# Optimization experiments

Measured on AMD Instinct MI355X. Metric: run time of the kernel, lower is better.

## Reference

```python
import jax, jax.numpy as jnp
import numpy as np

ALPHA = 1.0

def _soft_assign(x, clusters, alpha=ALPHA):
    # (avoids materializing the (N, K, D) broadcast intermediate)
    x_sq = jnp.sum(x * x, axis=1, keepdims=True)            # (N, 1)
    c_sq = jnp.sum(clusters * clusters, axis=1)             # (K,)
    cross = jnp.einsum('nd,kd->nk', x, clusters)            # (N, K)
    dist_sq = jnp.maximum(x_sq + c_sq[None, :] - 2.0 * cross, 0.0)
    q = 1.0 / (1.0 + dist_sq / alpha)
    q = q ** ((alpha + 1.0) / 2.0)
    return q / jnp.sum(q, axis=1, keepdims=True)            # row-normalize

def setup_inputs() -> dict:
    key = jax.random.key(0)
    k1, k2 = jax.random.split(key)
    N, D, K = 65536, 512, 1024
    x = jax.random.normal(k1, (N, D), dtype=jnp.float32)
    # xavier_uniform for (K, D): limit = sqrt(6 / (K + D))
    limit = float(np.sqrt(6.0 / (K + D)))
    clusters = jax.random.uniform(k2, (K, D), dtype=jnp.float32, minval=-limit, maxval=limit)
    return {"x": x, "clusters": clusters}

def reference(x, clusters):
    return _soft_assign(x, clusters)
```

## Files before the change

kernel.cpp:

```cpp
#include <hip/hip_runtime.h>

typedef __bf16 bf16x8 __attribute__((ext_vector_type(8)));
typedef float f32x16 __attribute__((ext_vector_type(16)));

__device__ __forceinline__ unsigned short f2bf(float f) {
    unsigned int u = __float_as_uint(f);
    u += 0x7FFFu + ((u >> 16) & 1u);
    return (unsigned short)(u >> 16);
}

__global__ __launch_bounds__(256) void prep_clusters(
    const float* __restrict__ cl, unsigned short* __restrict__ cbf,
    float* __restrict__ csq) {
    const int row  = blockIdx.x * 4 + (threadIdx.x >> 6);
    const int lane = threadIdx.x & 63;
    const float4* cg = (const float4*)(cl + ((size_t)row << 9));
    float ssq = 0.f;
#pragma unroll
    for (int i = 0; i < 2; ++i) {
        float4 v = cg[lane + 64 * i];
        ssq += v.x * v.x + v.y * v.y + v.z * v.z + v.w * v.w;
        ushort4 h;
        h.x = f2bf(v.x); h.y = f2bf(v.y); h.z = f2bf(v.z); h.w = f2bf(v.w);
        *(ushort4*)(cbf + ((size_t)row << 9) + (size_t)(lane + 64 * i) * 4) = h;
    }
#pragma unroll
    for (int off = 32; off >= 1; off >>= 1) ssq += __shfl_xor(ssq, off);
    if (lane == 0) csq[row] = ssq;
}

#define LDA 272

__global__ __launch_bounds__(1024, 4) void soft_assign(
    const float* __restrict__ x, const unsigned short* __restrict__ cbf,
    const float* __restrict__ csq, float* __restrict__ out) {
    __shared__ unsigned short xs[64 * LDA];
    __shared__ float part[64 * 32];
    __shared__ float xsq[64];
    __shared__ float inv[64];

    const int t    = threadIdx.x;
    const int lane = t & 63;
    const int w    = t >> 6;
    const int l31  = lane & 31;
    const int half = lane >> 5;
    const int rb   = blockIdx.x;

    part[t] = 0.f;
    part[t + 1024] = 0.f;

    const int col0   = w * 64 + l31;
    const float csq0 = csq[col0];
    const float csq1 = csq[col0 + 32];

    f32x16 c00, c01, c10, c11;
#pragma unroll
    for (int i = 0; i < 16; ++i) { c00[i] = 0.f; c01[i] = 0.f; c10[i] = 0.f; c11[i] = 0.f; }

    const int srow = t >> 4;
    const int sj   = t & 15;
    float ssq = 0.f;

    const unsigned short* b0base = cbf + (size_t)col0 * 512 + half * 8;
    const unsigned short* b1base = b0base + 32 * 512;
    const unsigned short* a0base = xs + l31 * LDA + half * 8;
    const unsigned short* a1base = a0base + 32 * LDA;

#pragma unroll 1
    for (int ch = 0; ch < 2; ++ch) {
        if (ch) __syncthreads();
        {
            const float4* xg = (const float4*)(x + (size_t)(rb * 64 + srow) * 512 + ch * 256);
#pragma unroll
            for (int i = 0; i < 4; ++i) {
                float4 v = xg[sj + 16 * i];
                ssq += v.x * v.x + v.y * v.y + v.z * v.z + v.w * v.w;
                ushort4 h;
                h.x = f2bf(v.x); h.y = f2bf(v.y); h.z = f2bf(v.z); h.w = f2bf(v.w);
                *(ushort4*)(xs + srow * LDA + (sj + 16 * i) * 4) = h;
            }
        }
        if (ch == 1) {
            float s2 = ssq;
#pragma unroll
            for (int off = 8; off >= 1; off >>= 1) s2 += __shfl_xor(s2, off);
            if (sj == 0) xsq[srow] = s2;
        }
        __syncthreads();

        const unsigned short* bp0 = b0base + ch * 256;
        const unsigned short* bp1 = b1base + ch * 256;
        bf16x8 b0 = *(const bf16x8*)bp0;
        bf16x8 b1 = *(const bf16x8*)bp1;
#pragma unroll 4
        for (int s = 0; s < 16; ++s) {
            const int nx = ((s + 1) & 15) * 16;
            bf16x8 b0n = *(const bf16x8*)(bp0 + nx);
            bf16x8 b1n = *(const bf16x8*)(bp1 + nx);
            bf16x8 a0 = *(const bf16x8*)(a0base + s * 16);
            bf16x8 a1 = *(const bf16x8*)(a1base + s * 16);
            c00 = __builtin_amdgcn_mfma_f32_32x32x16_bf16(a0, b0, c00, 0, 0, 0);
            c01 = __builtin_amdgcn_mfma_f32_32x32x16_bf16(a0, b1, c01, 0, 0, 0);
            c10 = __builtin_amdgcn_mfma_f32_32x32x16_bf16(a1, b0, c10, 0, 0, 0);
            c11 = __builtin_amdgcn_mfma_f32_32x32x16_bf16(a1, b1, c11, 0, 0, 0);
            b0 = b0n; b1 = b1n;
        }
    }

#pragma unroll
    for (int r = 0; r < 16; ++r) {
        const int rl0 = (r & 3) + 8 * (r >> 2) + 4 * half;
        const float x0 = xsq[rl0];
        const float x1 = xsq[rl0 + 32];
        float q00 = __builtin_amdgcn_rcpf(1.f + fmaxf(x0 + csq0 - 2.f * c00[r], 0.f));
        float q01 = __builtin_amdgcn_rcpf(1.f + fmaxf(x0 + csq1 - 2.f * c01[r], 0.f));
        float q10 = __builtin_amdgcn_rcpf(1.f + fmaxf(x1 + csq0 - 2.f * c10[r], 0.f));
        float q11 = __builtin_amdgcn_rcpf(1.f + fmaxf(x1 + csq1 - 2.f * c11[r], 0.f));
        c00[r] = q00; c01[r] = q01; c10[r] = q10; c11[r] = q11;
        atomicAdd(&part[rl0 * 32 + l31], q00 + q01);
        atomicAdd(&part[(rl0 + 32) * 32 + l31], q10 + q11);
    }
    __syncthreads();
    if (t < 64) {
        float s = 0.f;
#pragma unroll
        for (int c = 0; c < 32; ++c) s += part[t * 32 + c];
        inv[t] = __builtin_amdgcn_rcpf(s);
    }
    __syncthreads();

    float* og = out + (size_t)rb * 64 * 1024;
#pragma unroll
    for (int r = 0; r < 16; ++r) {
        const int rl0 = (r & 3) + 8 * (r >> 2) + 4 * half;
        const float i0 = inv[rl0];
        const float i1 = inv[rl0 + 32];
        og[(size_t)rl0 * 1024 + col0]             = c00[r] * i0;
        og[(size_t)rl0 * 1024 + col0 + 32]        = c01[r] * i0;
        og[(size_t)(rl0 + 32) * 1024 + col0]      = c10[r] * i1;
        og[(size_t)(rl0 + 32) * 1024 + col0 + 32] = c11[r] * i1;
    }
}

extern "C" void kernel_launch(void* const* d_in, const int* in_sizes, int n_in,
                              void* d_out, int out_size, void* d_ws, size_t ws_size,
                              hipStream_t stream) {
    const float* x  = (const float*)d_in[0];
    const float* cl = (const float*)d_in[1];
    float* out = (float*)d_out;

    unsigned short* cbf = (unsigned short*)d_ws;
    float* csq = (float*)((char*)d_ws + (size_t)1024 * 512 * 2);

    prep_clusters<<<256, 256, 0, stream>>>(cl, cbf, csq);
    soft_assign<<<1024, 1024, 0, stream>>>(x, cbf, csq, out);
}
```

Baseline: 630.0 us.

## Pre-swizzle bf16 operands into MFMA fragment order for contiguous lane loads

Cluster bf16 data is written in MFMA fragment-tiled order so each lane's B fragment is a contiguous 16-byte load and a wavefront reads one coalesced 1 KB block. The x tile in LDS is stored in the same fragment order, which drops the padded row stride. The MFMA loop is rewritten to prefetch B fragments two k-steps ahead. The x row sums of squares now use LDS atomics, and the final row-sum reduction is rotated to avoid bank conflicts. Costs include more atomics and a different bank-access pattern on the LDS fragment reads.

Result: faster. 570.1 us (-9.5%).

```diff
diff --git a/kernel.cpp b/kernel.cpp
--- a/kernel.cpp
+++ b/kernel.cpp
@@ -2,6 +2,7 @@
 
 typedef __bf16 bf16x8 __attribute__((ext_vector_type(8)));
 typedef float f32x16 __attribute__((ext_vector_type(16)));
+typedef unsigned short ushort8 __attribute__((ext_vector_type(8)));
 
 __device__ __forceinline__ unsigned short f2bf(float f) {
     unsigned int u = __float_as_uint(f);
@@ -14,27 +15,25 @@
     float* __restrict__ csq) {
     const int row  = blockIdx.x * 4 + (threadIdx.x >> 6);
     const int lane = threadIdx.x & 63;
-    const float4* cg = (const float4*)(cl + ((size_t)row << 9));
-    float ssq = 0.f;
-#pragma unroll
-    for (int i = 0; i < 2; ++i) {
-        float4 v = cg[lane + 64 * i];
-        ssq += v.x * v.x + v.y * v.y + v.z * v.z + v.w * v.w;
-        ushort4 h;
-        h.x = f2bf(v.x); h.y = f2bf(v.y); h.z = f2bf(v.z); h.w = f2bf(v.w);
-        *(ushort4*)(cbf + ((size_t)row << 9) + (size_t)(lane + 64 * i) * 4) = h;
-    }
+    const float4* cg = (const float4*)(cl + ((size_t)row << 9) + lane * 8);
+    float4 v0 = cg[0], v1 = cg[1];
+    float ssq = v0.x*v0.x + v0.y*v0.y + v0.z*v0.z + v0.w*v0.w
+              + v1.x*v1.x + v1.y*v1.y + v1.z*v1.z + v1.w*v1.w;
+    ushort8 h;
+    h[0]=f2bf(v0.x); h[1]=f2bf(v0.y); h[2]=f2bf(v0.z); h[3]=f2bf(v0.w);
+    h[4]=f2bf(v1.x); h[5]=f2bf(v1.y); h[6]=f2bf(v1.z); h[7]=f2bf(v1.w);
+    const int n = row & 31, T = row >> 5;
+    const int s = lane >> 1, hh = lane & 1;
+    *(ushort8*)(cbf + (size_t)((T * 32 + s) * 64 + hh * 32 + n) * 8) = h;
 #pragma unroll
     for (int off = 32; off >= 1; off >>= 1) ssq += __shfl_xor(ssq, off);
     if (lane == 0) csq[row] = ssq;
 }
 
-#define LDA 272
-
 __global__ __launch_bounds__(1024, 4) void soft_assign(
     const float* __restrict__ x, const unsigned short* __restrict__ cbf,
     const float* __restrict__ csq, float* __restrict__ out) {
-    __shared__ unsigned short xs[64 * LDA];
+    __shared__ unsigned short xs[2048 * 8];
     __shared__ float part[64 * 32];
     __shared__ float xsq[64];
     __shared__ float inv[64];
@@ -48,6 +47,7 @@
 
     part[t] = 0.f;
     part[t + 1024] = 0.f;
+    if (t < 64) xsq[t] = 0.f;
 
     const int col0   = w * 64 + l31;
     const float csq0 = csq[col0];
@@ -57,53 +57,60 @@
 #pragma unroll
     for (int i = 0; i < 16; ++i) { c00[i] = 0.f; c01[i] = 0.f; c10[i] = 0.f; c11[i] = 0.f; }
 
-    const int srow = t >> 4;
-    const int sj   = t & 15;
-    float ssq = 0.f;
+    const unsigned short* bT0 = cbf + ((size_t)(2 * w) * 32 * 64 + lane) * 8;
+    const unsigned short* bT1 = cbf + ((size_t)(2 * w + 1) * 32 * 64 + lane) * 8;
+    const unsigned short* aB  = xs + lane * 8;
 
-    const unsigned short* b0base = cbf + (size_t)col0 * 512 + half * 8;
-    const unsigned short* b1base = b0base + 32 * 512;
-    const unsigned short* a0base = xs + l31 * LDA + half * 8;
-    const unsigned short* a1base = a0base + 32 * LDA;
+    bf16x8 b0c = *(const bf16x8*)(bT0);
+    bf16x8 b1c = *(const bf16x8*)(bT1);
+    bf16x8 b0n = *(const bf16x8*)(bT0 + 512);
+    bf16x8 b1n = *(const bf16x8*)(bT1 + 512);
 
 #pragma unroll 1
     for (int ch = 0; ch < 2; ++ch) {
         if (ch) __syncthreads();
-        {
-            const float4* xg = (const float4*)(x + (size_t)(rb * 64 + srow) * 512 + ch * 256);
 #pragma unroll
-            for (int i = 0; i < 4; ++i) {
-                float4 v = xg[sj + 16 * i];
-                ssq += v.x * v.x + v.y * v.y + v.z * v.z + v.w * v.w;
-                ushort4 h;
-                h.x = f2bf(v.x); h.y = f2bf(v.y); h.z = f2bf(v.z); h.w = f2bf(v.w);
-                *(ushort4*)(xs + srow * LDA + (sj + 16 * i) * 4) = h;
-            }
-        }
-        if (ch == 1) {
-            float s2 = ssq;
-#pragma unroll
-            for (int off = 8; off >= 1; off >>= 1) s2 += __shfl_xor(s2, off);
-            if (sj == 0) xsq[srow] = s2;
+        for (int i = 0; i < 2; ++i) {
+            const int g  = 2 * t + i;
+            const int l  = g & 63;
+            const int sl = (g >> 6) & 15;
+            const int mt = g >> 10;
+            const int row = mt * 32 + (l & 31);
+            const int d0  = ch * 256 + sl * 16 + (l >> 5) * 8;
+            const float4* xg = (const float4*)(x + (size_t)(rb * 64 + row) * 512 + d0);
+            float4 v0 = xg[0], v1 = xg[1];
+            ushort8 h;
+            h[0]=f2bf(v0.x); h[1]=f2bf(v0.y); h[2]=f2bf(v0.z); h[3]=f2bf(v0.w);
+            h[4]=f2bf(v1.x); h[5]=f2bf(v1.y); h[6]=f2bf(v1.z); h[7]=f2bf(v1.w);
+            *(ushort8*)(xs + (size_t)g * 8) = h;
+            float ss = v0.x*v0.x + v0.y*v0.y + v0.z*v0.z + v0.w*v0.w
+                     + v1.x*v1.x + v1.y*v1.y + v1.z*v1.z + v1.w*v1.w;
+            atomicAdd(&xsq[row], ss);
         }
         __syncthreads();
 
-        const unsigned short* bp0 = b0base + ch * 256;
-        const unsigned short* bp1 = b1base + ch * 256;
-        bf16x8 b0 = *(const bf16x8*)bp0;
-        bf16x8 b1 = *(const bf16x8*)bp1;
-#pragma unroll 4
-        for (int s = 0; s < 16; ++s) {
-            const int nx = ((s + 1) & 15) * 16;
-            bf16x8 b0n = *(const bf16x8*)(bp0 + nx);
-            bf16x8 b1n = *(const bf16x8*)(bp1 + nx);
-            bf16x8 a0 = *(const bf16x8*)(a0base + s * 16);
-            bf16x8 a1 = *(const bf16x8*)(a1base + s * 16);
-            c00 = __builtin_amdgcn_mfma_f32_32x32x16_bf16(a0, b0, c00, 0, 0, 0);
-            c01 = __builtin_amdgcn_mfma_f32_32x32x16_bf16(a0, b1, c01, 0, 0, 0);
-            c10 = __builtin_amdgcn_mfma_f32_32x32x16_bf16(a1, b0, c10, 0, 0, 0);
-            c11 = __builtin_amdgcn_mfma_f32_32x32x16_bf16(a1, b1, c11, 0, 0, 0);
-            b0 = b0n; b1 = b1n;
+#pragma unroll 1
+        for (int sl = 0; sl < 16; sl += 2) {
+            const int sg  = ch * 16 + sl;
+            const int sp2 = (sg + 2) & 31;
+            const int sp3 = (sg + 3) & 31;
+            bf16x8 p0 = *(const bf16x8*)(bT0 + sp2 * 512);
+            bf16x8 p1 = *(const bf16x8*)(bT1 + sp2 * 512);
+            bf16x8 q0 = *(const bf16x8*)(bT0 + sp3 * 512);
+            bf16x8 q1 = *(const bf16x8*)(bT1 + sp3 * 512);
+            bf16x8 a0 = *(const bf16x8*)(aB + (sl)     * 512);
+            bf16x8 a1 = *(const bf16x8*)(aB + 8192 + (sl)     * 512);
+            bf16x8 a2 = *(const bf16x8*)(aB + (sl + 1) * 512);
+            bf16x8 a3 = *(const bf16x8*)(aB + 8192 + (sl + 1) * 512);
+            c00 = __builtin_amdgcn_mfma_f32_32x32x16_bf16(a0, b0c, c00, 0, 0, 0);
+            c01 = __builtin_amdgcn_mfma_f32_32x32x16_bf16(a0, b1c, c01, 0, 0, 0);
+            c10 = __builtin_amdgcn_mfma_f32_32x32x16_bf16(a1, b0c, c10, 0, 0, 0);
+            c11 = __builtin_amdgcn_mfma_f32_32x32x16_bf16(a1, b1c, c11, 0, 0, 0);
+            c00 = __builtin_amdgcn_mfma_f32_32x32x16_bf16(a2, b0n, c00, 0, 0, 0);
+            c01 = __builtin_amdgcn_mfma_f32_32x32x16_bf16(a2, b1n, c01, 0, 0, 0);
+            c10 = __builtin_amdgcn_mfma_f32_32x32x16_bf16(a3, b0n, c10, 0, 0, 0);
+            c11 = __builtin_amdgcn_mfma_f32_32x32x16_bf16(a3, b1n, c11, 0, 0, 0);
+            b0c = p0; b1c = p1; b0n = q0; b1n = q1;
         }
     }
 
@@ -124,7 +131,7 @@
     if (t < 64) {
         float s = 0.f;
 #pragma unroll
-        for (int c = 0; c < 32; ++c) s += part[t * 32 + c];
+        for (int c = 0; c < 32; ++c) s += part[t * 32 + ((c + t) & 31)];
         inv[t] = __builtin_amdgcn_rcpf(s);
     }
     __syncthreads();
```
